# Optimization experiments

Hardware: AMD Instinct MI355X
Metric: run time of the kernel (lower is better)

Reference implementation:

```python
import jax, jax.numpy as jnp
import numpy as np


def setup_inputs() -> dict:
    key = jax.random.key(0)
    k1, k2 = jax.random.split(key)
    x = jax.random.normal(k1, (4, 4096, 1024), dtype=jnp.float32)
    codebook = jax.random.normal(k2, (16384, 1024), dtype=jnp.float32)
    return {"x": x, "codebook": codebook}


def reference(x, codebook):
    # Euclidean snap: argmin over pairwise L2 distances, then gather.
    # Squared distances suffice for argmin (monotone transform of cdist p=2).
    x2 = jnp.sum(x * x, axis=-1, keepdims=True)            # [b, n, 1]
    c2 = jnp.sum(codebook * codebook, axis=-1)             # [c]
    xc = jnp.einsum('bnd,cd->bnc', x, codebook)            # [b, n, c]
    d2 = x2 - 2.0 * xc + c2                                # [b, n, c]
    codebook_ids = jnp.argmin(d2, axis=-1)                 # [b, n]
    output = jnp.take(codebook, codebook_ids, axis=0)      # [b, n, d]
    return output
```

## Files before the change

### kernel.cpp

```cpp
#include <hip/hip_runtime.h>
#include <hip/hip_bf16.h>
#include <stdint.h>

#define NROWS  16384
#define NCODES 16384
#define DIM    1024
#define NT     16
#define TCH    2048
#define MARGIN_Q 52

typedef float f32x4  __attribute__((ext_vector_type(4)));
typedef short bf16x8 __attribute__((ext_vector_type(8)));

__device__ __forceinline__ ushort f2bf(float f) {
  uint32_t u = __float_as_uint(f);
  uint32_t r = u + 0x7FFFu + ((u >> 16) & 1u);
  return (ushort)(r >> 16);
}
__device__ __forceinline__ int imin(int a, int b){ return a < b ? a : b; }
__device__ __forceinline__ int imax(int a, int b){ return a < b ? b : a; }
__device__ __forceinline__ int packKey32(float s, int idx) {
  int q = (int)rintf(s * 16.0f);
  return q * 16384 + idx;
}

#define GLDS16(gp, lp) \
  __builtin_amdgcn_global_load_lds((const __attribute__((address_space(1))) void*)(gp), \
                                   (__attribute__((address_space(3))) void*)(lp), 16, 0, 0)

__device__ __forceinline__ void sbar() {
  asm volatile("" ::: "memory");
  __builtin_amdgcn_s_barrier();
  asm volatile("" ::: "memory");
}

__global__ __launch_bounds__(256) void c2_kernel(const float* __restrict__ cb,
                                                 float* __restrict__ c2) {
  const int code = blockIdx.x;
  const int t = threadIdx.x, lane = t & 63, wid = t >> 6;
  f32x4 v = *(const f32x4*)(cb + (size_t)code * DIM + t * 4);
  float s = v[0]*v[0] + v[1]*v[1] + v[2]*v[2] + v[3]*v[3];
  #pragma unroll
  for (int off = 32; off; off >>= 1) s += __shfl_down(s, off);
  __shared__ float part[4];
  if (lane == 0) part[wid] = s;
  __syncthreads();
  if (t == 0) c2[code] = part[0] + part[1] + part[2] + part[3];
}

__global__ __launch_bounds__(256) void convert_swz256(const float* __restrict__ src,
                                                      ushort* __restrict__ dst) {
  const int chunk = blockIdx.x * 256 + threadIdx.x;
  const int pc  = chunk & 2047;
  const int kt  = (chunk >> 11) & 15;
  const int m   = chunk >> 15;
  const int row = pc >> 3;
  const int g   = (pc & 7) ^ (row & 7);
  const float* s = src + (size_t)(m * 256 + row) * DIM + kt * 64 + g * 8;
  f32x4 a0 = *(const f32x4*)s;
  f32x4 a1 = *(const f32x4*)(s + 4);
  bf16x8 p;
  #pragma unroll
  for (int j = 0; j < 4; ++j) {
    p[j]     = (short)f2bf(a0[j]);
    p[j + 4] = (short)f2bf(a1[j]);
  }
  *(bf16x8*)(dst + (size_t)chunk * 8) = p;
}


#define STAGE_A(BUF, KT, H) do {                                                  \
    GLDS16(ga + ((KT)*16384 + (H)*8192),        &lsA[BUF][(H)*8192 + w*512]);     \
    GLDS16(ga + ((KT)*16384 + (H)*8192 + 4096), &lsA[BUF][(H)*8192 + w*512 + 4096]); \
  } while (0)
#define STAGE_B(BUF, KT, H) do {                                                  \
    GLDS16(gb + ((KT)*16384 + (H)*8192),        &lsB[BUF][(H)*8192 + w*512]);     \
    GLDS16(gb + ((KT)*16384 + (H)*8192 + 4096), &lsB[BUF][(H)*8192 + w*512 + 4096]); \
  } while (0)

#define RD_A(MIB, BUF) do {                                                       \
    _Pragma("unroll")                                                             \
    for (int mi_ = 0; mi_ < 4; ++mi_) {                                           \
      aF[mi_][0] = *(const bf16x8*)(A0[BUF] + ((MIB) + mi_) * 1024);              \
      aF[mi_][1] = *(const bf16x8*)(A1[BUF] + ((MIB) + mi_) * 1024);              \
    } } while (0)
#define RD_Bx(DST, NIB, BUF) do {                                                 \
    _Pragma("unroll")                                                             \
    for (int ni_ = 0; ni_ < 2; ++ni_) {                                           \
      DST[ni_][0] = *(const bf16x8*)(B0[BUF] + ((NIB) + ni_) * 1024);             \
      DST[ni_][1] = *(const bf16x8*)(B1[BUF] + ((NIB) + ni_) * 1024);             \
    } } while (0)

#define MMA_Q(MB, NB, AF, BF) do {                                                \
    __builtin_amdgcn_s_setprio(1);                                                \
    _Pragma("unroll")                                                             \
    for (int ks_ = 0; ks_ < 2; ++ks_) {                                           \
      _Pragma("unroll")                                                           \
      for (int mi_ = 0; mi_ < 4; ++mi_) {                                         \
        _Pragma("unroll")                                                         \
        for (int ni_ = 0; ni_ < 2; ++ni_)                                         \
          acc[(MB) + mi_][(NB) + ni_] = __builtin_amdgcn_mfma_f32_16x16x32_bf16(  \
              AF[mi_][ks_], BF[ni_][ks_], acc[(MB) + mi_][(NB) + ni_], 0, 0, 0);  \
      } }                                                                         \
    __builtin_amdgcn_s_setprio(0);                                                \
  } while (0)

#define G8  asm volatile("s_waitcnt vmcnt(8)" ::: "memory")
#define G0  asm volatile("s_waitcnt vmcnt(0)" ::: "memory")
#define NOG do {} while (0)

#define TILE(KT, AC, BC, AN, BN_, DOST, GUARD) do {                               \
    RD_Bx(bF0, 0, BC);                                                            \
    RD_Bx(bF1, 2, BC);                                                            \
    asm volatile("s_waitcnt lgkmcnt(0)" ::: "memory");                            \
    sbar();                                                        \
    if (DOST) { STAGE_A(AN, (KT) + 2, 0); STAGE_A(AN, (KT) + 2, 1);               \
                STAGE_B(BN_, (KT) + 2, 0); STAGE_B(BN_, (KT) + 2, 1); }           \
    RD_A(0, AC);                                                                  \
    MMA_Q(0, 0, aF, bF0);                                                         \
    MMA_Q(0, 2, aF, bF1);                                                         \
    RD_A(4, AC);                                                                  \
    MMA_Q(4, 0, aF, bF0);                                                         \
    MMA_Q(4, 2, aF, bF1);                                                         \
    asm volatile("s_waitcnt lgkmcnt(0)" ::: "memory");                            \
    GUARD;                                                                        \
    sbar();                                                        \
  } while (0)

__global__ __launch_bounds__(512, 2) void snap_gemm256(const ushort* __restrict__ xs,
                                                       const ushort* __restrict__ cs,
                                                       const float* __restrict__ c2,
                                                       int* __restrict__ cand) {
  __shared__ ushort lsA[3][16384];
  __shared__ ushort lsB[2][16384];

  const int t    = threadIdx.x;
  const int lane = t & 63;
  const int w    = t >> 6;
  const int wm   = w >> 2;
  const int wn   = w & 3;
  const int l15  = lane & 15;
  const int kgrp = lane >> 4;

  const int bid = blockIdx.x;
  const int swz = (bid & 7) * 512 + (bid >> 3);
  const int bm  = swz & 63;
  const int bn  = swz >> 6;

  const ushort* xbase = xs + (size_t)bm * (16 * TCH) * 8;
  const ushort* cbase = cs + (size_t)bn * (16 * TCH) * 8;
  const ushort* ga = xbase + w * 512 + lane * 8;
  const ushort* gb = cbase + w * 512 + lane * 8;

  const int sw0  = ( kgrp      ^ (l15 & 7)) * 8;
  const int sw1  = ((4 | kgrp) ^ (l15 & 7)) * 8;
  const int arow = (wm * 128 + l15) * 64;
  const int brow = (wn * 64  + l15) * 64;
  const ushort* A0[3]; const ushort* A1[3];
  const ushort* B0[2]; const ushort* B1[2];
  #pragma unroll
  for (int b = 0; b < 3; ++b) { A0[b] = &lsA[b][arow + sw0]; A1[b] = &lsA[b][arow + sw1]; }
  #pragma unroll
  for (int b = 0; b < 2; ++b) { B0[b] = &lsB[b][brow + sw0]; B1[b] = &lsB[b][brow + sw1]; }

  f32x4 acc[8][4];
  #pragma unroll
  for (int mi = 0; mi < 8; ++mi)
    #pragma unroll
    for (int ni = 0; ni < 4; ++ni)
      acc[mi][ni] = (f32x4){0.f, 0.f, 0.f, 0.f};

  bf16x8 aF[4][2], bF0[2][2], bF1[2][2];

  STAGE_A(0, 0, 0); STAGE_A(0, 0, 1);
  STAGE_B(0, 0, 0); STAGE_B(0, 0, 1);
  STAGE_A(1, 1, 0); STAGE_A(1, 1, 1);
  STAGE_B(1, 1, 0); STAGE_B(1, 1, 1);
  G8;
  sbar();

  TILE(0 , 0, 0, 2, 0, 1, G8);
  TILE(1 , 1, 1, 0, 1, 1, G8);
  TILE(2 , 2, 0, 1, 0, 1, G8);
  TILE(3 , 0, 1, 2, 1, 1, G8);
  TILE(4 , 1, 0, 0, 0, 1, G8);
  TILE(5 , 2, 1, 1, 1, 1, G8);
  TILE(6 , 0, 0, 2, 0, 1, G8);
  TILE(7 , 1, 1, 0, 1, 1, G8);
  TILE(8 , 2, 0, 1, 0, 1, G8);
  TILE(9 , 0, 1, 2, 1, 1, G8);
  TILE(10, 1, 0, 0, 0, 1, G8);
  TILE(11, 2, 1, 1, 1, 1, G8);
  TILE(12, 0, 0, 2, 0, 1, G8);
  TILE(13, 1, 1, 0, 1, 1, G8);
  TILE(14, 2, 0, 1, 0, 0, G0);
  TILE(15, 0, 1, 2, 1, 0, NOG);

  __syncthreads();

  int* red = (int*)&lsA[0][0];
  float c2v[4];
  int   colv[4];
  #pragma unroll
  for (int ni = 0; ni < 4; ++ni) {
    colv[ni] = bn * 256 + wn * 64 + ni * 16 + l15;
    c2v[ni]  = c2[colv[ni]];
  }

  #pragma unroll
  for (int mi = 0; mi < 8; ++mi) {
    #pragma unroll
    for (int r = 0; r < 4; ++r) {
      int a = packKey32(fmaf(-2.0f, acc[mi][0][r], c2v[0]), colv[0]);
      int b = packKey32(fmaf(-2.0f, acc[mi][1][r], c2v[1]), colv[1]);
      int c = packKey32(fmaf(-2.0f, acc[mi][2][r], c2v[2]), colv[2]);
      int d = packKey32(fmaf(-2.0f, acc[mi][3][r], c2v[3]), colv[3]);
      int lo1 = imin(a, b), hi1 = imax(a, b);
      int lo2 = imin(c, d), hi2 = imax(c, d);
      int k1 = imin(lo1, lo2);
      int k2 = imin(imax(lo1, lo2), imin(hi1, hi2));
      #pragma unroll
      for (int m = 1; m < 16; m <<= 1) {
        int o1 = __shfl_xor(k1, m);
        int o2 = __shfl_xor(k2, m);
        int n1 = imin(k1, o1);
        int n2 = imin(imax(k1, o1), imin(k2, o2));
        k1 = n1; k2 = n2;
      }
      if (l15 == 0) {
        int rl = wm * 128 + mi * 16 + kgrp * 4 + r;
        red[(wn * 256 + rl) * 2 + 0] = k1;
        red[(wn * 256 + rl) * 2 + 1] = k2;
      }
    }
  }
  __syncthreads();

  if (t < 256) {
    int k1 = red[(0 * 256 + t) * 2 + 0];
    int k2 = red[(0 * 256 + t) * 2 + 1];
    #pragma unroll
    for (int q = 1; q < 4; ++q) {
      int p1 = red[(q * 256 + t) * 2 + 0];
      int p2 = red[(q * 256 + t) * 2 + 1];
      int n1 = imin(k1, p1);
      int n2 = imin(imax(k1, p1), imin(k2, p2));
      k1 = n1; k2 = n2;
    }
    size_t o = (size_t)(bm * 256 + t) * 128 + (size_t)bn * 2;
    cand[o]     = k1;
    cand[o + 1] = k2;
  }
}

__global__ __launch_bounds__(256) void snap_gemm_slow(const float* __restrict__ x,
                                                      const float* __restrict__ cb,
                                                      const float* __restrict__ c2,
                                                      int* __restrict__ cand) {
  __shared__ ushort lsA[2][8192];
  __shared__ ushort lsB[2][8192];
  __shared__ int redbuf[2][128][2];

  const int t    = threadIdx.x;
  const int lane = t & 63;
  const int wid  = t >> 6;
  const int wm   = wid & 1;
  const int wn   = wid >> 1;
  const int l15  = lane & 15;
  const int kgrp = lane >> 4;

  const int bm = blockIdx.x & 127;
  const int bn = blockIdx.x >> 7;
  const int rowBase = bm * 128;
  const int colBase = bn * 128;

  const float* aptr[4];
  const float* bptr[4];
  int ldsOff[4];
  #pragma unroll
  for (int i = 0; i < 4; ++i) {
    int pc = t + 256 * i;
    int row = pc >> 3;
    int g = (pc & 7) ^ (row & 7);
    aptr[i] = x  + (size_t)(rowBase + row) * DIM + g * 8;
    bptr[i] = cb + (size_t)(colBase + row) * DIM + g * 8;
    ldsOff[i] = pc * 8;
  }

  f32x4 acc[4][4];
  #pragma unroll
  for (int mi = 0; mi < 4; ++mi)
    #pragma unroll
    for (int ni = 0; ni < 4; ++ni)
      acc[mi][ni] = (f32x4){0.f, 0.f, 0.f, 0.f};

  auto STAGE = [&](int buf, int kt) {
    const int kOff = kt * 64;
    #pragma unroll
    for (int i = 0; i < 4; ++i) {
      f32x4 a0 = *(const f32x4*)(aptr[i] + kOff);
      f32x4 a1 = *(const f32x4*)(aptr[i] + kOff + 4);
      f32x4 b0 = *(const f32x4*)(bptr[i] + kOff);
      f32x4 b1 = *(const f32x4*)(bptr[i] + kOff + 4);
      bf16x8 pa, pb;
      #pragma unroll
      for (int j = 0; j < 4; ++j) {
        pa[j]     = (short)f2bf(a0[j]);
        pa[j + 4] = (short)f2bf(a1[j]);
        pb[j]     = (short)f2bf(b0[j]);
        pb[j + 4] = (short)f2bf(b1[j]);
      }
      *(bf16x8*)(&lsA[buf][ldsOff[i]]) = pa;
      *(bf16x8*)(&lsB[buf][ldsOff[i]]) = pb;
    }
  };

  STAGE(0, 0);
  __syncthreads();

  for (int kt = 0; kt < DIM / 64; ++kt) {
    const int cur = kt & 1;
    if (kt < DIM / 64 - 1) STAGE(cur ^ 1, kt + 1);

    const ushort* bA = &lsA[cur][0];
    const ushort* bB = &lsB[cur][0];
    #pragma unroll
    for (int ks = 0; ks < 2; ++ks) {
      const int gidx = ks * 4 + kgrp;
      bf16x8 af[4], bfr[4];
      #pragma unroll
      for (int mi = 0; mi < 4; ++mi) {
        int r_ = wm * 64 + mi * 16 + l15;
        af[mi] = *(const bf16x8*)(bA + (r_ * 8 + (gidx ^ (r_ & 7))) * 8);
      }
      #pragma unroll
      for (int ni = 0; ni < 4; ++ni) {
        int c_ = wn * 64 + ni * 16 + l15;
        bfr[ni] = *(const bf16x8*)(bB + (c_ * 8 + (gidx ^ (c_ & 7))) * 8);
      }
      #pragma unroll
      for (int mi = 0; mi < 4; ++mi)
        #pragma unroll
        for (int ni = 0; ni < 4; ++ni)
          acc[mi][ni] = __builtin_amdgcn_mfma_f32_16x16x32_bf16(af[mi], bfr[ni], acc[mi][ni], 0, 0, 0);
    }
    __syncthreads();
  }

  float c2v[4];
  int   colv[4];
  #pragma unroll
  for (int ni = 0; ni < 4; ++ni) {
    colv[ni] = colBase + wn * 64 + ni * 16 + l15;
    c2v[ni]  = c2[colv[ni]];
  }

  #pragma unroll
  for (int mi = 0; mi < 4; ++mi) {
    #pragma unroll
    for (int r = 0; r < 4; ++r) {
      int a = packKey32(fmaf(-2.0f, acc[mi][0][r], c2v[0]), colv[0]);
      int b = packKey32(fmaf(-2.0f, acc[mi][1][r], c2v[1]), colv[1]);
      int c = packKey32(fmaf(-2.0f, acc[mi][2][r], c2v[2]), colv[2]);
      int d = packKey32(fmaf(-2.0f, acc[mi][3][r], c2v[3]), colv[3]);
      int lo1 = imin(a, b), hi1 = imax(a, b);
      int lo2 = imin(c, d), hi2 = imax(c, d);
      int k1 = imin(lo1, lo2);
      int k2 = imin(imax(lo1, lo2), imin(hi1, hi2));
      #pragma unroll
      for (int m = 1; m < 16; m <<= 1) {
        int o1 = __shfl_xor(k1, m);
        int o2 = __shfl_xor(k2, m);
        int n1 = imin(k1, o1);
        int n2 = imin(imax(k1, o1), imin(k2, o2));
        k1 = n1; k2 = n2;
      }
      if (l15 == 0) {
        int rl = wm * 64 + mi * 16 + kgrp * 4 + r;
        redbuf[wn][rl][0] = k1;
        redbuf[wn][rl][1] = k2;
      }
    }
  }
  __syncthreads();

  if (t < 128) {
    int a1 = redbuf[0][t][0], a2 = redbuf[0][t][1];
    int b1 = redbuf[1][t][0], b2 = redbuf[1][t][1];
    int m1 = imin(a1, b1);
    int m2 = imin(imax(a1, b1), imin(a2, b2));
    size_t o = (size_t)(rowBase + t) * 256 + (size_t)bn * 2;
    cand[o]     = m1;
    cand[o + 1] = m2;
  }
}

__global__ __launch_bounds__(256) void rerank(const float* __restrict__ x,
                                              const float* __restrict__ cb,
                                              const int* __restrict__ cand,
                                              int* __restrict__ bestidx,
                                              int poolN) {
  const int row = blockIdx.x;
  const int t = threadIdx.x, lane = t & 63, wid = t >> 6;
  __shared__ int    smin[4];
  __shared__ int    gshared;
  __shared__ double dpart[4];
  __shared__ int    cnt;
  __shared__ int    list[64];

  int my = (t < poolN) ? cand[(size_t)row * poolN + t] : 0x7FFFFFFF;
  int k = my;
  #pragma unroll
  for (int off = 32; off; off >>= 1) k = imin(k, __shfl_down(k, off));
  if (lane == 0) smin[wid] = k;
  if (t == 0) cnt = 0;
  __syncthreads();
  if (t == 0) {
    int g = smin[0];
    for (int i = 1; i < 4; ++i) g = imin(g, smin[i]);
    gshared = g;
  }
  __syncthreads();

  const int gq = gshared >> 14;
  if ((my >> 14) <= gq + MARGIN_Q) {
    int p = atomicAdd(&cnt, 1);
    if (p < 64) list[p] = my & 16383;
  }
  __syncthreads();
  int n = cnt; if (n > 64) n = 64;

  uint64_t best = ~0ull;
  const float* xr = x + (size_t)row * DIM;
  for (int i = 0; i < n; ++i) {
    const int cidx = list[i];
    const float* cr = cb + (size_t)cidx * DIM;
    double p = 0.0;
    #pragma unroll
    for (int j = 0; j < 4; ++j) {
      int d = t + 256 * j;
      double diff = (double)xr[d] - (double)cr[d];
      p += diff * diff;
    }
    #pragma unroll
    for (int off = 32; off; off >>= 1) p += __shfl_down(p, off);
    if (lane == 0) dpart[wid] = p;
    __syncthreads();
    if (t == 0) {
      double d2 = dpart[0] + dpart[1] + dpart[2] + dpart[3];
      uint64_t bits = (uint64_t)__double_as_longlong(d2);
      uint64_t key = (bits & ~0x3FFFull) | (uint32_t)cidx;
      if (key < best) best = key;
    }
    __syncthreads();
  }
  if (t == 0) bestidx[row] = (int)(best & 0x3FFFull);
}

__global__ __launch_bounds__(256) void gather_rows(const float* __restrict__ cb,
                                                   const int* __restrict__ bestidx,
                                                   float* __restrict__ out) {
  const int row = blockIdx.x;
  const int idx = bestidx[row];
  f32x4 v = *(const f32x4*)(cb + (size_t)idx * DIM + threadIdx.x * 4);
  *(f32x4*)(out + (size_t)row * DIM + threadIdx.x * 4) = v;
}

extern "C" void kernel_launch(void* const* d_in, const int* in_sizes, int n_in,
                              void* d_out, int out_size, void* d_ws, size_t ws_size,
                              hipStream_t stream) {
  const float* x  = (const float*)d_in[0];
  const float* cb = (const float*)d_in[1];
  float* out = (float*)d_out;

  float* c2      = (float*)d_ws;
  int*   bestidx = (int*)((char*)d_ws + 64 * 1024);

  const size_t candBytes = (size_t)NROWS * 128 * 4;
  const size_t needFast  = 128 * 1024 + candBytes;

  c2_kernel<<<NCODES, 256, 0, stream>>>(cb, c2);

  if (ws_size >= needFast) {
    ushort* xs = (ushort*)d_out;
    ushort* cs = xs + (size_t)NROWS * DIM;
    int* cand = (int*)((char*)d_ws + 128 * 1024);

    convert_swz256<<<8192, 256, 0, stream>>>(x,  xs);
    convert_swz256<<<8192, 256, 0, stream>>>(cb, cs);
    snap_gemm256<<<4096, 512, 0, stream>>>(xs, cs, c2, cand);
    rerank<<<NROWS, 256, 0, stream>>>(x, cb, cand, bestidx, 128);
    gather_rows<<<NROWS, 256, 0, stream>>>(cb, bestidx, out);
  } else {
    int* cand = (int*)d_out;
    snap_gemm_slow<<<(NROWS / 128) * (NCODES / 128), 256, 0, stream>>>(x, cb, c2, cand);
    rerank<<<NROWS, 256, 0, stream>>>(x, cb, cand, bestidx, 256);
    gather_rows<<<NROWS, 256, 0, stream>>>(cb, bestidx, out);
  }
}
```

Before: 650.8 us.

## Switch candidate-search GEMM from bf16 to fp8 MFMA with wider rerank margin

Converts x and the codebook to fp8 e4m3 in a new swizzled layout and runs the distance GEMM with fp8 MFMA instructions, halving the bytes staged through LDS per k-tile and doubling MFMA throughput. The candidate margin is widened so the exact fp32 rerank can still recover the true nearest code despite the coarser scores. The risks are more candidates passing the margin, which raises rerank cost, and possible misses if fp8 error exceeds the margin.

```diff
diff --git a/kernel.cpp b/kernel.cpp
--- a/kernel.cpp
+++ b/kernel.cpp
@@ -1,16 +1,17 @@
 #include <hip/hip_runtime.h>
 #include <hip/hip_bf16.h>
+#include <hip/hip_fp8.h>
 #include <stdint.h>
 
 #define NROWS  16384
 #define NCODES 16384
 #define DIM    1024
 #define NT     16
-#define TCH    2048
-#define MARGIN_Q 52
+#define MARGIN_Q 514
 
 typedef float f32x4  __attribute__((ext_vector_type(4)));
 typedef short bf16x8 __attribute__((ext_vector_type(8)));
+typedef unsigned char uchar;
 
 __device__ __forceinline__ ushort f2bf(float f) {
   uint32_t u = __float_as_uint(f);
@@ -48,47 +49,50 @@
   if (t == 0) c2[code] = part[0] + part[1] + part[2] + part[3];
 }
 
-__global__ __launch_bounds__(256) void convert_swz256(const float* __restrict__ src,
-                                                      ushort* __restrict__ dst) {
+__global__ __launch_bounds__(256) void convert_fp8_swz(const float* __restrict__ src,
+                                                       uchar* __restrict__ dst) {
   const int chunk = blockIdx.x * 256 + threadIdx.x;
-  const int pc  = chunk & 2047;
-  const int kt  = (chunk >> 11) & 15;
-  const int m   = chunk >> 15;
-  const int row = pc >> 3;
-  const int g   = (pc & 7) ^ (row & 7);
-  const float* s = src + (size_t)(m * 256 + row) * DIM + kt * 64 + g * 8;
-  f32x4 a0 = *(const f32x4*)s;
-  f32x4 a1 = *(const f32x4*)(s + 4);
-  bf16x8 p;
-  #pragma unroll
-  for (int j = 0; j < 4; ++j) {
-    p[j]     = (short)f2bf(a0[j]);
-    p[j + 4] = (short)f2bf(a1[j]);
-  }
-  *(bf16x8*)(dst + (size_t)chunk * 8) = p;
-}
-
-
-#define STAGE_A(BUF, KT, H) do {                                                  \
-    GLDS16(ga + ((KT)*16384 + (H)*8192),        &lsA[BUF][(H)*8192 + w*512]);     \
-    GLDS16(ga + ((KT)*16384 + (H)*8192 + 4096), &lsA[BUF][(H)*8192 + w*512 + 4096]); \
+  const int p   = chunk & 3;
+  const int row = (chunk >> 2) & 255;
+  const int kt  = (chunk >> 10) & 15;
+  const int m   = chunk >> 14;
+  const int c   = p ^ ((row & 7) >> 1);
+  const float* s = src + (size_t)(m * 256 + row) * DIM + kt * 64 + c * 16;
+  uchar b[16];
+  #pragma unroll
+  for (int j = 0; j < 16; ++j) {
+    __hip_fp8_e4m3 h(s[j]);
+    b[j] = h.__x;
+  }
+  uint64_t lo = 0, hi = 0;
+  #pragma unroll
+  for (int j = 0; j < 8; ++j) { lo |= (uint64_t)b[j] << (8 * j); hi |= (uint64_t)b[j + 8] << (8 * j); }
+  uint64_t* o = (uint64_t*)(dst + (size_t)chunk * 16);
+  if (row & 1) { o[0] = hi; o[1] = lo; }
+  else         { o[0] = lo; o[1] = hi; }
+}
+
+
+#define STAGE_A(BUF, KT) do {                                                     \
+    GLDS16(ga + (KT)*16384,        &lsA[BUF][w*1024]);                            \
+    GLDS16(ga + (KT)*16384 + 8192, &lsA[BUF][w*1024 + 8192]);                     \
   } while (0)
-#define STAGE_B(BUF, KT, H) do {                                                  \
-    GLDS16(gb + ((KT)*16384 + (H)*8192),        &lsB[BUF][(H)*8192 + w*512]);     \
-    GLDS16(gb + ((KT)*16384 + (H)*8192 + 4096), &lsB[BUF][(H)*8192 + w*512 + 4096]); \
+#define STAGE_B(BUF, KT) do {                                                     \
+    GLDS16(gb + (KT)*16384,        &lsB[BUF][w*1024]);                            \
+    GLDS16(gb + (KT)*16384 + 8192, &lsB[BUF][w*1024 + 8192]);                     \
   } while (0)
 
 #define RD_A(MIB, BUF) do {                                                       \
     _Pragma("unroll")                                                             \
     for (int mi_ = 0; mi_ < 4; ++mi_) {                                           \
-      aF[mi_][0] = *(const bf16x8*)(A0[BUF] + ((MIB) + mi_) * 1024);              \
-      aF[mi_][1] = *(const bf16x8*)(A1[BUF] + ((MIB) + mi_) * 1024);              \
+      aF[mi_][0] = *(const long*)(A0[BUF] + ((MIB) + mi_) * 1024);                \
+      aF[mi_][1] = *(const long*)(A1[BUF] + ((MIB) + mi_) * 1024);                \
     } } while (0)
 #define RD_Bx(DST, NIB, BUF) do {                                                 \
     _Pragma("unroll")                                                             \
     for (int ni_ = 0; ni_ < 2; ++ni_) {                                           \
-      DST[ni_][0] = *(const bf16x8*)(B0[BUF] + ((NIB) + ni_) * 1024);             \
-      DST[ni_][1] = *(const bf16x8*)(B1[BUF] + ((NIB) + ni_) * 1024);             \
+      DST[ni_][0] = *(const long*)(B0[BUF] + ((NIB) + ni_) * 1024);               \
+      DST[ni_][1] = *(const long*)(B1[BUF] + ((NIB) + ni_) * 1024);               \
     } } while (0)
 
 #define MMA_Q(MB, NB, AF, BF) do {                                                \
@@ -99,13 +103,13 @@
       for (int mi_ = 0; mi_ < 4; ++mi_) {                                         \
         _Pragma("unroll")                                                         \
         for (int ni_ = 0; ni_ < 2; ++ni_)                                         \
-          acc[(MB) + mi_][(NB) + ni_] = __builtin_amdgcn_mfma_f32_16x16x32_bf16(  \
+          acc[(MB) + mi_][(NB) + ni_] = __builtin_amdgcn_mfma_f32_16x16x32_fp8_fp8( \
               AF[mi_][ks_], BF[ni_][ks_], acc[(MB) + mi_][(NB) + ni_], 0, 0, 0);  \
       } }                                                                         \
     __builtin_amdgcn_s_setprio(0);                                                \
   } while (0)
 
-#define G8  asm volatile("s_waitcnt vmcnt(8)" ::: "memory")
+#define G4  asm volatile("s_waitcnt vmcnt(4)" ::: "memory")
 #define G0  asm volatile("s_waitcnt vmcnt(0)" ::: "memory")
 #define NOG do {} while (0)
 
@@ -114,8 +118,7 @@
     RD_Bx(bF1, 2, BC);                                                            \
     asm volatile("s_waitcnt lgkmcnt(0)" ::: "memory");                            \
     sbar();                                                        \
-    if (DOST) { STAGE_A(AN, (KT) + 2, 0); STAGE_A(AN, (KT) + 2, 1);               \
-                STAGE_B(BN_, (KT) + 2, 0); STAGE_B(BN_, (KT) + 2, 1); }           \
+    if (DOST) { STAGE_A(AN, (KT) + 2); STAGE_B(BN_, (KT) + 2); }                  \
     RD_A(0, AC);                                                                  \
     MMA_Q(0, 0, aF, bF0);                                                         \
     MMA_Q(0, 2, aF, bF1);                                                         \
@@ -127,12 +130,12 @@
     sbar();                                                        \
   } while (0)
 
-__global__ __launch_bounds__(512, 2) void snap_gemm256(const ushort* __restrict__ xs,
-                                                       const ushort* __restrict__ cs,
+__global__ __launch_bounds__(512, 2) void snap_gemm256(const uchar* __restrict__ xs,
+                                                       const uchar* __restrict__ cs,
                                                        const float* __restrict__ c2,
                                                        int* __restrict__ cand) {
-  __shared__ ushort lsA[3][16384];
-  __shared__ ushort lsB[2][16384];
+  __shared__ uchar lsA[3][16384];
+  __shared__ uchar lsB[2][16384];
 
   const int t    = threadIdx.x;
   const int lane = t & 63;
@@ -147,17 +150,15 @@
   const int bm  = swz & 63;
   const int bn  = swz >> 6;
 
-  const ushort* xbase = xs + (size_t)bm * (16 * TCH) * 8;
-  const ushort* cbase = cs + (size_t)bn * (16 * TCH) * 8;
-  const ushort* ga = xbase + w * 512 + lane * 8;
-  const ushort* gb = cbase + w * 512 + lane * 8;
-
-  const int sw0  = ( kgrp      ^ (l15 & 7)) * 8;
-  const int sw1  = ((4 | kgrp) ^ (l15 & 7)) * 8;
+  const uchar* ga = xs + (size_t)bm * 16 * 16384 + w * 1024 + lane * 16;
+  const uchar* gb = cs + (size_t)bn * 16 * 16384 + w * 1024 + lane * 16;
+
+  const int sw0  = (( kgrp)      ^ (l15 & 7)) * 8;
+  const int sw1  = ((4 | kgrp)   ^ (l15 & 7)) * 8;
   const int arow = (wm * 128 + l15) * 64;
   const int brow = (wn * 64  + l15) * 64;
-  const ushort* A0[3]; const ushort* A1[3];
-  const ushort* B0[2]; const ushort* B1[2];
+  const uchar* A0[3]; const uchar* A1[3];
+  const uchar* B0[2]; const uchar* B1[2];
   #pragma unroll
   for (int b = 0; b < 3; ++b) { A0[b] = &lsA[b][arow + sw0]; A1[b] = &lsA[b][arow + sw1]; }
   #pragma unroll
@@ -170,29 +171,27 @@
     for (int ni = 0; ni < 4; ++ni)
       acc[mi][ni] = (f32x4){0.f, 0.f, 0.f, 0.f};
 
-  bf16x8 aF[4][2], bF0[2][2], bF1[2][2];
-
-  STAGE_A(0, 0, 0); STAGE_A(0, 0, 1);
-  STAGE_B(0, 0, 0); STAGE_B(0, 0, 1);
-  STAGE_A(1, 1, 0); STAGE_A(1, 1, 1);
-  STAGE_B(1, 1, 0); STAGE_B(1, 1, 1);
-  G8;
+  long aF[4][2], bF0[2][2], bF1[2][2];
+
+  STAGE_A(0, 0); STAGE_B(0, 0);
+  STAGE_A(1, 1); STAGE_B(1, 1);
+  G4;
   sbar();
 
-  TILE(0 , 0, 0, 2, 0, 1, G8);
-  TILE(1 , 1, 1, 0, 1, 1, G8);
-  TILE(2 , 2, 0, 1, 0, 1, G8);
-  TILE(3 , 0, 1, 2, 1, 1, G8);
-  TILE(4 , 1, 0, 0, 0, 1, G8);
-  TILE(5 , 2, 1, 1, 1, 1, G8);
-  TILE(6 , 0, 0, 2, 0, 1, G8);
-  TILE(7 , 1, 1, 0, 1, 1, G8);
-  TILE(8 , 2, 0, 1, 0, 1, G8);
-  TILE(9 , 0, 1, 2, 1, 1, G8);
-  TILE(10, 1, 0, 0, 0, 1, G8);
-  TILE(11, 2, 1, 1, 1, 1, G8);
-  TILE(12, 0, 0, 2, 0, 1, G8);
-  TILE(13, 1, 1, 0, 1, 1, G8);
+  TILE(0 , 0, 0, 2, 0, 1, G4);
+  TILE(1 , 1, 1, 0, 1, 1, G4);
+  TILE(2 , 2, 0, 1, 0, 1, G4);
+  TILE(3 , 0, 1, 2, 1, 1, G4);
+  TILE(4 , 1, 0, 0, 0, 1, G4);
+  TILE(5 , 2, 1, 1, 1, 1, G4);
+  TILE(6 , 0, 0, 2, 0, 1, G4);
+  TILE(7 , 1, 1, 0, 1, 1, G4);
+  TILE(8 , 2, 0, 1, 0, 1, G4);
+  TILE(9 , 0, 1, 2, 1, 1, G4);
+  TILE(10, 1, 0, 0, 0, 1, G4);
+  TILE(11, 2, 1, 1, 1, 1, G4);
+  TILE(12, 0, 0, 2, 0, 1, G4);
+  TILE(13, 1, 1, 0, 1, 1, G4);
   TILE(14, 2, 0, 1, 0, 0, G0);
   TILE(15, 0, 1, 2, 1, 0, NOG);
 
@@ -482,12 +481,12 @@
   c2_kernel<<<NCODES, 256, 0, stream>>>(cb, c2);
 
   if (ws_size >= needFast) {
-    ushort* xs = (ushort*)d_out;
-    ushort* cs = xs + (size_t)NROWS * DIM;
+    uchar* xs = (uchar*)d_out;
+    uchar* cs = xs + (size_t)NROWS * DIM;
     int* cand = (int*)((char*)d_ws + 128 * 1024);
 
-    convert_swz256<<<8192, 256, 0, stream>>>(x,  xs);
-    convert_swz256<<<8192, 256, 0, stream>>>(cb, cs);
+    convert_fp8_swz<<<4096, 256, 0, stream>>>(x,  xs);
+    convert_fp8_swz<<<4096, 256, 0, stream>>>(cb, cs);
     snap_gemm256<<<4096, 512, 0, stream>>>(xs, cs, c2, cand);
     rerank<<<NROWS, 256, 0, stream>>>(x, cb, cand, bestidx, 128);
     gather_rows<<<NROWS, 256, 0, stream>>>(cb, bestidx, out);
```

New measurement: 645.2 us. Within noise of the previous version (-0.9%).
